# Kernel optimization log

Hardware: AMD Instinct MI355X
Metric: run time of the kernel (lower is better)

The kernel has to match this reference:

```python
import jax, jax.numpy as jnp
import numpy as np

# Configuration mirroring init_kwargs
B, H, W = 64, 40, 40          # batch, grid (image 1280 / stride 32)
A, C = 5, 80                  # anchors per cell, classes
MAX_BOXES = 100               # max_detection_boxes
SCORE_THR = 0.001             # nms_score_threshold
IOU_THR = 0.5                 # nms_iou_threshold


def setup_inputs() -> dict:
    key = jax.random.key(0)
    k1, k2 = jax.random.split(key)
    predictions = jax.random.normal(k1, (B, H, W, A * (5 + C)), dtype=jnp.float32)
    # anchor (w, h) in grid-cell units, positive
    anchors = jax.random.uniform(k2, (A, 2), dtype=jnp.float32, minval=0.5, maxval=8.0)
    return {"predictions": predictions, "anchors": anchors}


def decode_yolo(predictions, anchors):
    """YOLOv2-style decode -> normalized corner boxes and per-class scores."""
    b, h, w, _ = predictions.shape
    p = predictions.reshape(b, h, w, A, 5 + C)
    gy, gx = jnp.meshgrid(jnp.arange(h, dtype=jnp.float32),
                          jnp.arange(w, dtype=jnp.float32), indexing="ij")
    grid = jnp.stack([gx, gy], axis=-1)[None, :, :, None, :]   # [1,h,w,1,2]
    dims = jnp.array([w, h], dtype=jnp.float32)
    xy = (jax.nn.sigmoid(p[..., 0:2]) + grid) / dims           # normalized centers
    wh = jnp.exp(p[..., 2:4]) * anchors / dims                 # normalized sizes
    conf = jax.nn.sigmoid(p[..., 4:5])
    probs = jax.nn.softmax(p[..., 5:], axis=-1)
    scores = conf * probs                                      # [b,h,w,A,C]
    boxes = jnp.concatenate([xy - wh * 0.5, xy + wh * 0.5], axis=-1)  # x1,y1,x2,y2
    return boxes.reshape(b, -1, 4), scores.reshape(b, -1, C)


def nms_single(boxes, scores_all):
    """Greedy per-class NMS for one image. boxes [N,4], scores_all [N,C]."""
    cls_scores = jnp.max(scores_all, axis=-1)
    classes = jnp.argmax(scores_all, axis=-1)
    s0 = jnp.where(cls_scores > SCORE_THR, cls_scores, -1.0)
    area = jnp.maximum(boxes[:, 2] - boxes[:, 0], 0.0) * \
           jnp.maximum(boxes[:, 3] - boxes[:, 1], 0.0)

    def step(s, _):
        idx = jnp.argmax(s)
        sc = s[idx]
        box = boxes[idx]
        x1 = jnp.maximum(box[0], boxes[:, 0]); y1 = jnp.maximum(box[1], boxes[:, 1])
        x2 = jnp.minimum(box[2], boxes[:, 2]); y2 = jnp.minimum(box[3], boxes[:, 3])
        inter = jnp.maximum(x2 - x1, 0.0) * jnp.maximum(y2 - y1, 0.0)
        box_area = jnp.maximum(box[2] - box[0], 0.0) * jnp.maximum(box[3] - box[1], 0.0)
        iou = inter / (area + box_area - inter + 1e-8)
        suppress = (iou > IOU_THR) & (classes == classes[idx])
        s_new = jnp.where(suppress, -1.0, s).at[idx].set(-1.0)
        valid = sc > 0.0
        out_box = jnp.where(valid, box, 0.0)
        out_sc = jnp.where(valid, sc, 0.0)
        out_cl = jnp.where(valid, classes[idx], -1)
        return s_new, (out_box, out_sc, out_cl)

    _, (ob, osc, ocl) = jax.lax.scan(step, s0, None, length=MAX_BOXES)
    return ob, osc, ocl  # [MAX_BOXES,4], [MAX_BOXES], [MAX_BOXES]


def reference(predictions, anchors):
    boxes, scores = decode_yolo(predictions, anchors)
    sel_boxes, sel_scores, sel_classes = jax.vmap(nms_single)(boxes, scores)
    return sel_boxes, sel_scores, sel_classes
```

## Files before the change

### kernel.cpp

```cpp
#include <hip/hip_runtime.h>
#include <math.h>

#define B 64
#define H 40
#define W 40
#define A 5
#define C 80
#define NBOX (H*W*A)
#define FEAT (5+C)
#define MAXB 100
#define SCORE_THR 0.001f
#define IOU_THR 0.5f

#define DEC_THREADS 256

#define HBINS 10240
#define BINBASE 119808
#define TARGET 512

#define BK 48
#define RCAP 1024

typedef unsigned long long u64;
typedef unsigned int u32;

__global__ __launch_bounds__(DEC_THREADS) void decode_kernel(
    const float* __restrict__ pred, const float* __restrict__ anchors,
    float* __restrict__ boxes_ws, float* __restrict__ s_ws, int* __restrict__ cls_ws)
{
    const int box = blockIdx.x * DEC_THREADS + threadIdx.x;
    const float* __restrict__ r = pred + (long long)box * FEAT;

    float v[FEAT];
    #pragma unroll
    for (int i = 0; i < FEAT; ++i) v[i] = r[i];

    int img  = box / NBOX;
    int n    = box - img * NBOX;
    int cell = n / A;
    int a    = n - cell * A;
    int gx   = cell % W;
    int gy   = cell / W;

    float tx = v[0], ty = v[1], tw = v[2], th = v[3], tc = v[4];

    float sx = 1.f / (1.f + expf(-tx));
    float sy = 1.f / (1.f + expf(-ty));
    float cx = (sx + (float)gx) / (float)W;
    float cy = (sy + (float)gy) / (float)H;
    float aw = anchors[a*2+0], ah = anchors[a*2+1];
    float bw = expf(tw) * aw / (float)W;
    float bh = expf(th) * ah / (float)H;
    float conf = 1.f / (1.f + expf(-tc));

    float mm[8];
    #pragma unroll
    for (int w = 0; w < 8; ++w) mm[w] = v[5+w];
    #pragma unroll
    for (int i = 8; i < C; ++i) mm[i & 7] = fmaxf(mm[i & 7], v[5+i]);
    float m = fmaxf(fmaxf(fmaxf(mm[0],mm[1]),fmaxf(mm[2],mm[3])),
                    fmaxf(fmaxf(mm[4],mm[5]),fmaxf(mm[6],mm[7])));

    float sum = 0.f;
    float bv[4] = {-1.f,-1.f,-1.f,-1.f};
    int   bi[4] = {0,0,0,0};
    #pragma unroll
    for (int i = 0; i < C; ++i) {
        float e = expf(v[5+i] - m);
        sum += e;
        int w = i & 3;
        if (e > bv[w]) { bv[w] = e; bi[w] = i; }
    }
    float best_e = bv[0]; int best_c = bi[0];
    #pragma unroll
    for (int w = 1; w < 4; ++w) {
        if (bv[w] > best_e || (bv[w] == best_e && bi[w] < best_c)) { best_e = bv[w]; best_c = bi[w]; }
    }

    float score = conf * (best_e / sum);
    float s0 = (score > SCORE_THR) ? score : -1.0f;

    float x1 = cx - bw*0.5f, y1 = cy - bh*0.5f;
    float x2 = cx + bw*0.5f, y2 = cy + bh*0.5f;

    ((float4*)boxes_ws)[box] = make_float4(x1, y1, x2, y2);
    s_ws[box] = s0;
    cls_ws[box] = best_c;
}

__device__ __forceinline__ u64 wave_max_u64(u64 v) {
    #define STAGE(CTRL, RMASK) { \
        u32 lo = (u32)v, hi = (u32)(v >> 32); \
        u32 tlo = (u32)__builtin_amdgcn_update_dpp(0, (int)lo, CTRL, RMASK, 0xf, true); \
        u32 thi = (u32)__builtin_amdgcn_update_dpp(0, (int)hi, CTRL, RMASK, 0xf, true); \
        u64 t = ((u64)thi << 32) | (u64)tlo; \
        if (t > v) v = t; \
    }
    STAGE(0x111, 0xf)
    STAGE(0x112, 0xf)
    STAGE(0x114, 0xf)
    STAGE(0x118, 0xf)
    STAGE(0x142, 0xa)
    STAGE(0x143, 0xc)
    #undef STAGE
    u32 flo = (u32)__builtin_amdgcn_readlane((int)(u32)v, 63);
    u32 fhi = (u32)__builtin_amdgcn_readlane((int)(v >> 32), 63);
    return ((u64)fhi << 32) | (u64)flo;
}

__global__ __launch_bounds__(1024) void selnmsrank_kernel(
    const float* __restrict__ boxes_ws, const float* __restrict__ s_ws,
    const int* __restrict__ cls_ws, float* __restrict__ out)
{
    __shared__ __align__(16) char smem[HBINS * 4];
    int* hist  = (int*)smem;
    u64* bkey  = (u64*)smem;
    u64* ckeys = (u64*)(smem + 30720);
    int* bcnt  = (int*)(smem + 38912);
    __shared__ int wavesum[16];
    __shared__ int tbin_s;
    __shared__ int cnt;

    const int img  = blockIdx.x;
    const int tid  = threadIdx.x;
    const int lane = tid & 63;
    const int wid  = tid >> 6;
    const long long ib = (long long)img * NBOX;

    #pragma unroll
    for (int q = 0; q < HBINS/1024; ++q) hist[tid + q*1024] = 0;
    if (tid == 0) { tbin_s = 0; cnt = 0; }
    __syncthreads();

    float sc_r[8];
    #pragma unroll
    for (int k = 0; k < 8; ++k) {
        int j = tid + k*1024;
        float s = (j < NBOX) ? s_ws[ib + j] : -1.f;
        sc_r[k] = s;
        if (s > 0.f) {
            int b = (int)(__float_as_uint(s) >> 13) - BINBASE;
            b = max(0, min(HBINS-1, b));
            atomicAdd(&hist[b], 1);
        }
    }
    __syncthreads();

    int sum_r = 0;
    {
        int base = HBINS - 10*(tid+1);
        #pragma unroll
        for (int q = 0; q < 10; ++q) sum_r += hist[base + q];
    }
    int incl = sum_r;
    #pragma unroll
    for (int off = 1; off < 64; off <<= 1) {
        int o = __shfl_up(incl, off);
        if (lane >= off) incl += o;
    }
    if (lane == 63) wavesum[wid] = incl;
    __syncthreads();
    {
        int wbase = 0;
        for (int w = 0; w < wid; ++w) wbase += wavesum[w];
        int excl = wbase + incl - sum_r;
        if (excl < TARGET && excl + sum_r >= TARGET) {
            int cum = excl;
            for (int q = 0; q < 10; ++q) {
                int b = HBINS - 10*tid - 1 - q;
                cum += hist[b];
                if (cum >= TARGET) { tbin_s = b; break; }
            }
        }
    }
    __syncthreads();
    const int tb = tbin_s;

    if (tid < C) bcnt[tid] = 0;
    __syncthreads();

    #pragma unroll
    for (int k = 0; k < 8; ++k) {
        int j = tid + k*1024;
        float s = sc_r[k];
        if (j < NBOX && s > 0.f) {
            int b = (int)(__float_as_uint(s) >> 13) - BINBASE;
            b = max(0, min(HBINS-1, b));
            if (b >= tb) {
                int c = cls_ws[ib + j];
                int pos = atomicAdd(&bcnt[c], 1);
                if (pos < BK) {
                    u64 key = ((u64)__float_as_uint(s) << 32)
                            | ((u64)(NBOX - j) << 19)
                            | ((u64)pos << 13) | (u64)c;
                    bkey[c*BK + pos] = key;
                }
            }
        }
    }
    __syncthreads();

    for (int q = 0; q < 5; ++q) {
        const int c  = wid*5 + q;
        const int nb = min(bcnt[c], BK);

        u64 key = 0, keep = 0;
        float x1=0.f, y1=0.f, x2=0.f, y2=0.f, ar=0.f;
        if (lane < nb) {
            key = bkey[c*BK + lane];
            int bidx = NBOX - (int)((key >> 19) & 0x1FFF);
            float4 b4 = ((const float4*)boxes_ws)[ib + bidx];
            x1=b4.x; y1=b4.y; x2=b4.z; y2=b4.w;
            ar = fmaxf(x2-x1,0.f)*fmaxf(y2-y1,0.f);
        }

        for (int t = 0; t < BK; ++t) {
            u64 bk = wave_max_u64(key);
            if (bk == 0) break;
            int sl = (int)((bk >> 13) & 63);
            float sx1 = __shfl(x1, sl), sy1 = __shfl(y1, sl);
            float sx2 = __shfl(x2, sl), sy2 = __shfl(y2, sl);
            float sarea = fmaxf(sx2-sx1,0.f)*fmaxf(sy2-sy1,0.f);

            if (lane == sl) {
                keep = key;
                key = 0;
            } else if (key != 0) {
                float ix1 = fmaxf(sx1, x1);
                float iy1 = fmaxf(sy1, y1);
                float ix2 = fminf(sx2, x2);
                float iy2 = fminf(sy2, y2);
                float inter = fmaxf(ix2-ix1,0.f)*fmaxf(iy2-iy1,0.f);
                float iou = inter / (ar + sarea - inter + 1e-8f);
                if (iou > IOU_THR) key = 0;
            }
        }

        if (lane < BK) bkey[c*BK + lane] = keep;
    }
    __syncthreads();

    for (int i = tid; i < C*BK; i += 1024) {
        u64 k = bkey[i];
        if (k != 0) {
            int p = atomicAdd(&cnt, 1);
            if (p < RCAP) ckeys[p] = k;
        }
    }
    __syncthreads();
    const int m = min(cnt, RCAP);

    float* out_boxes  = out;
    float* out_scores = out + B*MAXB*4;
    float* out_cls    = out + B*MAXB*5;

    for (int i = tid; i < m; i += 1024) {
        u64 mine = ckeys[i];
        int r = 0;
        for (int j = 0; j < m; ++j) r += (ckeys[j] > mine) ? 1 : 0;
        if (r < MAXB) {
            int c    = (int)(mine & 127);
            int bidx = NBOX - (int)((mine >> 19) & 0x1FFF);
            float4 b4 = ((const float4*)boxes_ws)[ib + bidx];
            int o = img*MAXB + r;
            out_boxes[o*4+0] = b4.x; out_boxes[o*4+1] = b4.y;
            out_boxes[o*4+2] = b4.z; out_boxes[o*4+3] = b4.w;
            out_scores[o] = __uint_as_float((u32)(mine >> 32));
            out_cls[o]    = (float)c;
        }
    }

    int base = min(m, MAXB);
    for (int r = base + tid; r < MAXB; r += 1024) {
        int o = img*MAXB + r;
        out_boxes[o*4+0]=0.f; out_boxes[o*4+1]=0.f;
        out_boxes[o*4+2]=0.f; out_boxes[o*4+3]=0.f;
        out_scores[o]=0.f;
        out_cls[o]=-1.f;
    }
}

extern "C" void kernel_launch(void* const* d_in, const int* in_sizes, int n_in,
                              void* d_out, int out_size, void* d_ws, size_t ws_size,
                              hipStream_t stream) {
    const float* pred    = (const float*)d_in[0];
    const float* anchors = (const float*)d_in[1];
    float* out = (float*)d_out;

    char* p = (char*)d_ws;
    float*  boxes_ws  = (float*)p;              p += (size_t)B*NBOX*4*sizeof(float);
    float*  s_ws      = (float*)p;              p += (size_t)B*NBOX*sizeof(float);
    int*    cls_ws    = (int*)p;

    decode_kernel<<<(B*NBOX)/DEC_THREADS, DEC_THREADS, 0, stream>>>(
        pred, anchors, boxes_ws, s_ws, cls_ws);
    selnmsrank_kernel<<<B, 1024, 0, stream>>>(
        boxes_ws, s_ws, cls_ws, out);
}
```

Before: 285.7 us.

## Stage decode input tiles through LDS with async global-to-LDS loads

```diff
diff --git a/kernel.cpp b/kernel.cpp
--- a/kernel.cpp
+++ b/kernel.cpp
@@ -12,7 +12,10 @@
 #define SCORE_THR 0.001f
 #define IOU_THR 0.5f
 
-#define DEC_THREADS 256
+#define DEC_THREADS 64
+#define TILE_B4 1360
+#define NT 8000
+#define GRIDP 1792
 
 #define HBINS 10240
 #define BINBASE 119808
@@ -28,64 +31,95 @@
     const float* __restrict__ pred, const float* __restrict__ anchors,
     float* __restrict__ boxes_ws, float* __restrict__ s_ws, int* __restrict__ cls_ws)
 {
-    const int box = blockIdx.x * DEC_THREADS + threadIdx.x;
-    const float* __restrict__ r = pred + (long long)box * FEAT;
-
-    float v[FEAT];
-    #pragma unroll
-    for (int i = 0; i < FEAT; ++i) v[i] = r[i];
-
-    int img  = box / NBOX;
-    int n    = box - img * NBOX;
-    int cell = n / A;
-    int a    = n - cell * A;
-    int gx   = cell % W;
-    int gy   = cell / W;
-
-    float tx = v[0], ty = v[1], tw = v[2], th = v[3], tc = v[4];
-
-    float sx = 1.f / (1.f + expf(-tx));
-    float sy = 1.f / (1.f + expf(-ty));
-    float cx = (sx + (float)gx) / (float)W;
-    float cy = (sy + (float)gy) / (float)H;
-    float aw = anchors[a*2+0], ah = anchors[a*2+1];
-    float bw = expf(tw) * aw / (float)W;
-    float bh = expf(th) * ah / (float)H;
-    float conf = 1.f / (1.f + expf(-tc));
-
-    float mm[8];
-    #pragma unroll
-    for (int w = 0; w < 8; ++w) mm[w] = v[5+w];
-    #pragma unroll
-    for (int i = 8; i < C; ++i) mm[i & 7] = fmaxf(mm[i & 7], v[5+i]);
-    float m = fmaxf(fmaxf(fmaxf(mm[0],mm[1]),fmaxf(mm[2],mm[3])),
-                    fmaxf(fmaxf(mm[4],mm[5]),fmaxf(mm[6],mm[7])));
-
-    float sum = 0.f;
-    float bv[4] = {-1.f,-1.f,-1.f,-1.f};
-    int   bi[4] = {0,0,0,0};
-    #pragma unroll
-    for (int i = 0; i < C; ++i) {
-        float e = expf(v[5+i] - m);
-        sum += e;
-        int w = i & 3;
-        if (e > bv[w]) { bv[w] = e; bi[w] = i; }
-    }
-    float best_e = bv[0]; int best_c = bi[0];
-    #pragma unroll
-    for (int w = 1; w < 4; ++w) {
-        if (bv[w] > best_e || (bv[w] == best_e && bi[w] < best_c)) { best_e = bv[w]; best_c = bi[w]; }
-    }
-
-    float score = conf * (best_e / sum);
-    float s0 = (score > SCORE_THR) ? score : -1.0f;
-
-    float x1 = cx - bw*0.5f, y1 = cy - bh*0.5f;
-    float x2 = cx + bw*0.5f, y2 = cy + bh*0.5f;
-
-    ((float4*)boxes_ws)[box] = make_float4(x1, y1, x2, y2);
-    s_ws[box] = s0;
-    cls_ws[box] = best_c;
+    __shared__ float lds[1408 * 4];
+    const int tid = threadIdx.x;
+    const long long TOT4 = (long long)NT * TILE_B4;
+    const float4* src4 = (const float4*)pred;
+
+    auto stage = [&](int t) {
+        const long long base4 = (long long)t * TILE_B4;
+        #pragma unroll
+        for (int i = 0; i < 22; ++i) {
+            long long g4 = base4 + i*64 + tid;
+            if (g4 >= TOT4) g4 = TOT4 - 1;
+            __builtin_amdgcn_global_load_lds(
+                (const __attribute__((address_space(1))) void*)(src4 + g4),
+                (__attribute__((address_space(3))) void*)((char*)lds + i*1024),
+                16, 0, 0);
+        }
+    };
+
+    int t = blockIdx.x;
+    stage(t);
+
+    while (t < NT) {
+        __syncthreads();
+
+        float v[FEAT];
+        const float* l = lds + tid * FEAT;
+        #pragma unroll
+        for (int i = 0; i < FEAT; ++i) v[i] = l[i];
+
+        __syncthreads();
+
+        const int tn = t + GRIDP;
+        if (tn < NT) stage(tn);
+
+        const int box = t * DEC_THREADS + tid;
+        int img  = box / NBOX;
+        int n    = box - img * NBOX;
+        int cell = n / A;
+        int a    = n - cell * A;
+        int gx   = cell % W;
+        int gy   = cell / W;
+
+        float tx = v[0], ty = v[1], tw = v[2], th = v[3], tc = v[4];
+
+        float sx = 1.f / (1.f + expf(-tx));
+        float sy = 1.f / (1.f + expf(-ty));
+        float cx = (sx + (float)gx) / (float)W;
+        float cy = (sy + (float)gy) / (float)H;
+        float aw = anchors[a*2+0], ah = anchors[a*2+1];
+        float bw = expf(tw) * aw / (float)W;
+        float bh = expf(th) * ah / (float)H;
+        float conf = 1.f / (1.f + expf(-tc));
+
+        float mm[8];
+        #pragma unroll
+        for (int w = 0; w < 8; ++w) mm[w] = v[5+w];
+        #pragma unroll
+        for (int i = 8; i < C; ++i) mm[i & 7] = fmaxf(mm[i & 7], v[5+i]);
+        float m = fmaxf(fmaxf(fmaxf(mm[0],mm[1]),fmaxf(mm[2],mm[3])),
+                        fmaxf(fmaxf(mm[4],mm[5]),fmaxf(mm[6],mm[7])));
+
+        float sum = 0.f;
+        float bv[4] = {-1.f,-1.f,-1.f,-1.f};
+        int   bi[4] = {0,0,0,0};
+        #pragma unroll
+        for (int i = 0; i < C; ++i) {
+            float e = expf(v[5+i] - m);
+            sum += e;
+            int w = i & 3;
+            if (e > bv[w]) { bv[w] = e; bi[w] = i; }
+        }
+        float best_e = bv[0]; int best_c = bi[0];
+        #pragma unroll
+        for (int w = 1; w < 4; ++w) {
+            if (bv[w] > best_e || (bv[w] == best_e && bi[w] < best_c)) { best_e = bv[w]; best_c = bi[w]; }
+        }
+
+        float score = conf * (best_e / sum);
+        float s0 = (score > SCORE_THR) ? score : -1.0f;
+
+        float x1 = cx - bw*0.5f, y1 = cy - bh*0.5f;
+        float x2 = cx + bw*0.5f, y2 = cy + bh*0.5f;
+
+        ((float4*)boxes_ws)[box] = make_float4(x1, y1, x2, y2);
+        s_ws[box] = s0;
+        cls_ws[box] = best_c;
+
+        t = tn;
+    }
 }
 
 __device__ __forceinline__ u64 wave_max_u64(u64 v) {
@@ -292,7 +326,7 @@
     float*  s_ws      = (float*)p;              p += (size_t)B*NBOX*sizeof(float);
     int*    cls_ws    = (int*)p;
 
-    decode_kernel<<<(B*NBOX)/DEC_THREADS, DEC_THREADS, 0, stream>>>(
+    decode_kernel<<<GRIDP, DEC_THREADS, 0, stream>>>(
         pred, anchors, boxes_ws, s_ws, cls_ws);
     selnmsrank_kernel<<<B, 1024, 0, stream>>>(
         boxes_ws, s_ws, cls_ws, out);
```

Result: no change. 290.3 us (+1.6%).
